# Optimization experiments

Hardware: AMD Instinct MI355X
Metric: run time of the kernel (lower is better)

Reference implementation:

```python
import jax, jax.numpy as jnp
import numpy as np

D_MODEL = 1024
NHEAD = 16
HEAD_DIM = D_MODEL // NHEAD
MLP_DIM = 4096
ROPE_THETA = 10000.0


def layer_norm(x, g, b, eps=1e-5):
    mu = jnp.mean(x, axis=-1, keepdims=True)
    var = jnp.var(x, axis=-1, keepdims=True)
    return (x - mu) * jax.lax.rsqrt(var + eps) * g + b


def rope_cos_sin(seq_len, dim):
    # lucidrains RotaryEmbedding: inv_freq over even indices, freqs repeated interleaved
    inv_freq = 1.0 / (ROPE_THETA ** (jnp.arange(0, dim, 2, dtype=jnp.float32) / dim))
    t = jnp.arange(seq_len, dtype=jnp.float32)
    freqs = t[:, None] * inv_freq[None, :]            # (S, dim/2)
    freqs = jnp.repeat(freqs, 2, axis=-1)             # (S, dim) interleaved [f0,f0,f1,f1,...]
    return jnp.cos(freqs), jnp.sin(freqs)


def apply_rope(x, cos, sin):
    # x: (B, S, H, D); interleaved rotate_half: (x0,x1) -> (-x1, x0)
    x1 = x[..., ::2]
    x2 = x[..., 1::2]
    rot = jnp.stack([-x2, x1], axis=-1).reshape(x.shape)
    c = cos[None, :, None, :]
    s = sin[None, :, None, :]
    return x * c + rot * s


def setup_inputs() -> dict:
    key = jax.random.key(0)
    ks = jax.random.split(key, 8)
    B, S = 2, 2048
    sc = 1.0 / np.sqrt(D_MODEL)
    inputs = jax.random.normal(ks[0], (B, S, D_MODEL), dtype=jnp.float32)
    return {
        "inputs": inputs,
        "ln1_g": jnp.ones((D_MODEL,), jnp.float32),
        "ln1_b": jnp.zeros((D_MODEL,), jnp.float32),
        "Wq": jax.random.normal(ks[1], (D_MODEL, D_MODEL), jnp.float32) * sc,
        "Wk": jax.random.normal(ks[2], (D_MODEL, D_MODEL), jnp.float32) * sc,
        "Wv": jax.random.normal(ks[3], (D_MODEL, D_MODEL), jnp.float32) * sc,
        "Wo": jax.random.normal(ks[4], (D_MODEL, D_MODEL), jnp.float32) * sc,
        "ln2_g": jnp.ones((D_MODEL,), jnp.float32),
        "ln2_b": jnp.zeros((D_MODEL,), jnp.float32),
        "Wfc2": jax.random.normal(ks[5], (D_MODEL, MLP_DIM), jnp.float32) * sc,
        "bfc2": jnp.zeros((MLP_DIM,), jnp.float32),
        "Wfc3": jax.random.normal(ks[6], (MLP_DIM, D_MODEL), jnp.float32) * (1.0 / np.sqrt(MLP_DIM)),
        "bfc3": jnp.zeros((D_MODEL,), jnp.float32),
    }


def reference(inputs, ln1_g, ln1_b, Wq, Wk, Wv, Wo, ln2_g, ln2_b, Wfc2, bfc2, Wfc3, bfc3):
    B, S, _ = inputs.shape
    x = layer_norm(inputs, ln1_g, ln1_b)
    q = (x @ Wq).reshape(B, S, NHEAD, HEAD_DIM)
    k = (x @ Wk).reshape(B, S, NHEAD, HEAD_DIM)
    v = (x @ Wv).reshape(B, S, NHEAD, HEAD_DIM)
    cos, sin = rope_cos_sin(S, HEAD_DIM)
    q = apply_rope(q, cos, sin)
    k = apply_rope(k, cos, sin)
    scores = jnp.einsum('bqhd,bkhd->bhqk', q, k) / np.sqrt(HEAD_DIM)
    attn = jax.nn.softmax(scores, axis=-1)
    out = jnp.einsum('bhqk,bkhd->bqhd', attn, v).reshape(B, S, D_MODEL)
    out = out @ Wo
    mlp_in = out + inputs
    h = layer_norm(mlp_in, ln2_g, ln2_b)
    h = jax.nn.gelu(h @ Wfc2 + bfc2, approximate=False)
    h = h @ Wfc3 + bfc3
    return h + mlp_in
```

## Files before the change

### kernel.cpp

```cpp
#include <hip/hip_runtime.h>
#include <cstdint>
#include <cstddef>

typedef __bf16 bf16x8 __attribute__((ext_vector_type(8)));
typedef __bf16 bf16x4 __attribute__((ext_vector_type(4)));
typedef float  f32x4  __attribute__((ext_vector_type(4)));
typedef float  f32x16 __attribute__((ext_vector_type(16)));

__device__ __forceinline__ void load16_to_lds(const void* g, void* l) {
  __builtin_amdgcn_global_load_lds(
      (const __attribute__((address_space(1))) void*)g,
      (__attribute__((address_space(3))) void*)l, 16, 0, 0);
}

__global__ __launch_bounds__(256) void transpose_cast(
    const float* __restrict__ src, __bf16* __restrict__ dst, int K, int N)
{
  __shared__ float tile[32][33];
  const int n0 = blockIdx.x * 32, k0 = blockIdx.y * 32;
  const int tx = threadIdx.x, ty = threadIdx.y;
#pragma unroll
  for (int i = 0; i < 32; i += 8)
    tile[ty + i][tx] = src[(size_t)(k0 + ty + i) * N + n0 + tx];
  __syncthreads();
#pragma unroll
  for (int i = 0; i < 32; i += 8)
    dst[(size_t)(n0 + ty + i) * K + k0 + tx] = (__bf16)tile[tx][ty + i];
}

__global__ __launch_bounds__(256) void transpose_cast_qkv(
    const float* __restrict__ s0, const float* __restrict__ s1,
    const float* __restrict__ s2, __bf16* __restrict__ dst)
{
  __shared__ float tile[32][33];
  const float* src = blockIdx.z == 0 ? s0 : blockIdx.z == 1 ? s1 : s2;
  __bf16* d = dst + (size_t)blockIdx.z * 1024 * 1024;
  const int n0 = blockIdx.x * 32, k0 = blockIdx.y * 32;
  const int tx = threadIdx.x, ty = threadIdx.y;
#pragma unroll
  for (int i = 0; i < 32; i += 8)
    tile[ty + i][tx] = src[(size_t)(k0 + ty + i) * 1024 + n0 + tx];
  __syncthreads();
#pragma unroll
  for (int i = 0; i < 32; i += 8)
    d[(size_t)(n0 + ty + i) * 1024 + k0 + tx] = (__bf16)tile[tx][ty + i];
}

__global__ __launch_bounds__(256) void ln_kernel(
    const float* __restrict__ x, const float* __restrict__ g,
    const float* __restrict__ bta, __bf16* __restrict__ out)
{
  const int row = blockIdx.x;
  const int t = threadIdx.x;
  const float4 v = ((const float4*)(x + (size_t)row * 1024))[t];
  float s  = v.x + v.y + v.z + v.w;
  float ss = v.x * v.x + v.y * v.y + v.z * v.z + v.w * v.w;
#pragma unroll
  for (int o = 32; o > 0; o >>= 1) { s += __shfl_down(s, o); ss += __shfl_down(ss, o); }
  __shared__ float rs[4], rss[4];
  const int w = t >> 6, l = t & 63;
  if (l == 0) { rs[w] = s; rss[w] = ss; }
  __syncthreads();
  s  = rs[0] + rs[1] + rs[2] + rs[3];
  ss = rss[0] + rss[1] + rss[2] + rss[3];
  const float mu = s * (1.0f / 1024.0f);
  const float var = ss * (1.0f / 1024.0f) - mu * mu;
  const float rstd = rsqrtf(var + 1e-5f);
  const float4 gg = ((const float4*)g)[t];
  const float4 bb = ((const float4*)bta)[t];
  __bf16* o = out + (size_t)row * 1024 + t * 4;
  o[0] = (__bf16)((v.x - mu) * rstd * gg.x + bb.x);
  o[1] = (__bf16)((v.y - mu) * rstd * gg.y + bb.y);
  o[2] = (__bf16)((v.z - mu) * rstd * gg.z + bb.z);
  o[3] = (__bf16)((v.w - mu) * rstd * gg.w + bb.w);
}

enum { EPI_BF16 = 0, EPI_RES_F32 = 1, EPI_GELU_BF16 = 2, EPI_BIAS_RES_F32 = 3 };

template <int TM, int KB, int EPI>
__global__ __launch_bounds__(256, 2) void gemm_bf16(
    const __bf16* __restrict__ A, const __bf16* __restrict__ Bt,
    __bf16* __restrict__ outb, float* __restrict__ outf,
    const float* __restrict__ bias, const float* __restrict__ res,
    int M, int N, int K)
{
  constexpr int MT = TM / 32;
  constexpr int KS = KB / 32;
  __shared__ __bf16 As0[TM * KB], As1[TM * KB];
  __shared__ __bf16 Bs0[128 * KB], Bs1[128 * KB];
  const int tid  = threadIdx.x;
  const int lane = tid & 63, w = tid >> 6;
  const int wm = w >> 1, wn = w & 1;
  const int quad = lane >> 4, l16 = lane & 15;
  const int m0 = blockIdx.y * TM, n0 = blockIdx.x * 128;

  f32x4 acc[MT][4] = {};
  const __bf16* Ag = A  + (size_t)m0 * K;
  const __bf16* Bg = Bt + (size_t)n0 * K;

#define G_STAGE(AsX, BsX, k0) {                                            \
    _Pragma("unroll")                                                      \
    for (int r2 = 0; r2 < TM * KB / 2048; ++r2) {                          \
      const int c = r2 * 256 + tid;                                        \
      const int r = c / (KB / 8), cb = c % (KB / 8);                       \
      const int g = (KB == 64) ? (cb ^ (r & 7)) : cb;                      \
      load16_to_lds(Ag + (size_t)r * K + (k0) + g * 8, &AsX[c * 8]);       \
    }                                                                      \
    _Pragma("unroll")                                                      \
    for (int r2 = 0; r2 < KB / 16; ++r2) {                                 \
      const int c = r2 * 256 + tid;                                        \
      const int r = c / (KB / 8), cb = c % (KB / 8);                       \
      const int g = (KB == 64) ? (cb ^ (r & 7)) : cb;                      \
      load16_to_lds(Bg + (size_t)r * K + (k0) + g * 8, &BsX[c * 8]);       \
    } }

#define G_COMPUTE(AsX, BsX) {                                              \
    bf16x8 af[MT][KS], bfr[4][KS];                                         \
    _Pragma("unroll")                                                      \
    for (int mt = 0; mt < MT; ++mt) {                                      \
      const int row = wm * (TM / 2) + mt * 16 + l16;                       \
      _Pragma("unroll")                                                    \
      for (int ks = 0; ks < KS; ++ks) {                                    \
        const int ch = (KB == 64) ? ((ks * 4 + quad) ^ (row & 7)) : quad;  \
        af[mt][ks] = *(const bf16x8*)&AsX[row * KB + ch * 8];              \
      }                                                                    \
    }                                                                      \
    _Pragma("unroll")                                                      \
    for (int nt = 0; nt < 4; ++nt) {                                       \
      const int row = wn * 64 + nt * 16 + l16;                             \
      _Pragma("unroll")                                                    \
      for (int ks = 0; ks < KS; ++ks) {                                    \
        const int ch = (KB == 64) ? ((ks * 4 + quad) ^ (row & 7)) : quad;  \
        bfr[nt][ks] = *(const bf16x8*)&BsX[row * KB + ch * 8];             \
      }                                                                    \
    }                                                                      \
    _Pragma("unroll")                                                      \
    for (int ks = 0; ks < KS; ++ks)                                        \
      _Pragma("unroll")                                                    \
      for (int mt = 0; mt < MT; ++mt)                                      \
        _Pragma("unroll")                                                  \
        for (int nt = 0; nt < 4; ++nt)                                     \
          acc[mt][nt] = __builtin_amdgcn_mfma_f32_16x16x32_bf16(           \
              af[mt][ks], bfr[nt][ks], acc[mt][nt], 0, 0, 0);              \
  }

  G_STAGE(As0, Bs0, 0);
  const int nk = K / KB;
  for (int kt = 0; kt < nk; kt += 2) {
    __syncthreads();
    if (kt + 1 < nk) G_STAGE(As1, Bs1, (kt + 1) * KB);
    G_COMPUTE(As0, Bs0);
    __syncthreads();
    if (kt + 2 < nk) G_STAGE(As0, Bs0, (kt + 2) * KB);
    G_COMPUTE(As1, Bs1);
  }
#undef G_STAGE
#undef G_COMPUTE

#pragma unroll
  for (int mt = 0; mt < MT; ++mt) {
#pragma unroll
    for (int nt = 0; nt < 4; ++nt) {
      const int col = n0 + wn * 64 + nt * 16 + l16;
#pragma unroll
      for (int i = 0; i < 4; ++i) {
        const int row = m0 + wm * (TM / 2) + mt * 16 + quad * 4 + i;
        float v = acc[mt][nt][i];
        const size_t idx = (size_t)row * N + col;
        if (EPI == EPI_BF16) {
          outb[idx] = (__bf16)v;
        } else if (EPI == EPI_RES_F32) {
          outf[idx] = v + res[idx];
        } else if (EPI == EPI_GELU_BF16) {
          v += bias[col];
          outb[idx] = (__bf16)(0.5f * v * (1.0f + erff(v * 0.70710678118f)));
        } else {
          v += bias[col];
          outf[idx] = v + res[idx];
        }
      }
    }
  }
}

__global__ __launch_bounds__(256) void rope_qk(
    const __bf16* __restrict__ qkv, __bf16* __restrict__ qr, __bf16* __restrict__ kr)
{
  const int idx = blockIdx.x * 256 + threadIdx.x;
  const int d2 = idx & 31;
  const int h  = (idx >> 5) & 15;
  const int bs = idx >> 9;
  const int s  = bs & 2047;
  const int b  = bs >> 11;
  const float inv_freq = exp2f(-((float)d2 * (1.0f / 32.0f)) * 13.2877123795f);
  const float ang = (float)s * inv_freq;
  const float c = cosf(ang), sn = sinf(ang);
  const float QS = 0.125f * 1.44269504f;
  const __bf16* qp = qkv + (size_t)bs * 3072 + h * 64 + 2 * d2;
  const __bf16* kp = qp + 1024;
  const float q0 = (float)qp[0], q1 = (float)qp[1];
  const float k0 = (float)kp[0], k1 = (float)kp[1];
  const size_t o = ((size_t)(b * 16 + h) * 2048 + s) * 64 + 2 * d2;
  qr[o]     = (__bf16)((q0 * c - q1 * sn) * QS);
  qr[o + 1] = (__bf16)((q1 * c + q0 * sn) * QS);
  kr[o]     = (__bf16)(k0 * c - k1 * sn);
  kr[o + 1] = (__bf16)(k1 * c + k0 * sn);
}

__global__ __launch_bounds__(256) void v_transpose(
    const __bf16* __restrict__ qkv, __bf16* __restrict__ vt)
{
  __shared__ __bf16 t[64][72];
  const int st = blockIdx.x, h = blockIdx.y, b = blockIdx.z;
  const int tx = threadIdx.x & 63, ty = threadIdx.x >> 6;
  const int s0 = st * 64;
  const __bf16* src = qkv + ((size_t)(b * 2048 + s0)) * 3072 + 2048 + h * 64;
#pragma unroll
  for (int i = 0; i < 64; i += 4)
    t[ty + i][tx] = src[(size_t)(ty + i) * 3072 + tx];
  __syncthreads();
  __bf16* dst = vt + ((size_t)(b * 16 + h) * 64) * 2048 + s0;
#pragma unroll
  for (int i = 0; i < 64; i += 4)
    dst[(size_t)(ty + i) * 2048 + tx] = t[tx][ty + i];
}

__global__ __launch_bounds__(256, 2) void attn_kernel(
    const __bf16* __restrict__ qr, const __bf16* __restrict__ kr,
    const __bf16* __restrict__ vt, __bf16* __restrict__ attn_o)
{
  constexpr int S = 2048, DH = 64, NH = 16, BQ = 128, BKK = 64;
  __shared__ __align__(16) __bf16 Qs[BQ * 64];
  __shared__ __align__(16) __bf16 Ks0[64 * 64], Ks1[64 * 64];
  __shared__ __align__(16) __bf16 Vts0[64 * 64], Vts1[64 * 64];

  const int tid = threadIdx.x;
  const int lane = tid & 63, w = tid >> 6;
  const int l32 = lane & 31, half = lane >> 5;
  const int qt = blockIdx.x, h = blockIdx.y, b = blockIdx.z;
  const int bh = b * NH + h;
  const __bf16* Q  = qr + ((size_t)bh * S + qt * BQ) * DH;
  const __bf16* Kp = kr + (size_t)bh * S * DH;
  const __bf16* Vp = vt + (size_t)bh * DH * S;
  __bf16* Pb = Qs + w * 2048;

#define A_STAGE(KsX, VtsX, kk) {                                           \
    _Pragma("unroll")                                                      \
    for (int r2 = 0; r2 < 2; ++r2) {                                       \
      const int c = r2 * 256 + tid;                                        \
      const int r = c >> 3, cb = c & 7;                                    \
      const int cg = (cb ^ (r & 7)) * 8;                                   \
      load16_to_lds(Kp + (size_t)((kk) + r) * DH + cg, &KsX[c * 8]);       \
      load16_to_lds(Vp + (size_t)r * S + (kk) + cg, &VtsX[c * 8]);         \
    } }

#pragma unroll
  for (int r4 = 0; r4 < 4; ++r4) {
    const int c = r4 * 256 + tid;
    const int r = c >> 3, cb = c & 7;
    load16_to_lds(Q + (size_t)r * DH + ((cb ^ (r & 7)) * 8), &Qs[c * 8]);
  }
  A_STAGE(Ks0, Vts0, 0);
  __syncthreads();

  bf16x8 qfB[4];
  {
    const int row = w * 32 + l32;
#pragma unroll
    for (int c = 0; c < 4; ++c)
      qfB[c] = *(const bf16x8*)&Qs[row * 64 + (((2 * c + half) ^ (row & 7)) * 8)];
  }

  float mreg = -3.0e38f, lreg = 0.0f;
  f32x16 oacc[2] = {};

#define A_COMPUTE(KsX, VtsX) {                                             \
    bf16x8 kf[2][4], vf[2][4];                                             \
    _Pragma("unroll")                                                      \
    for (int t = 0; t < 2; ++t) {                                          \
      const int row = 32 * t + l32;                                        \
      _Pragma("unroll")                                                    \
      for (int c = 0; c < 4; ++c)                                          \
        kf[t][c] = *(const bf16x8*)&KsX[row * 64 + (((2 * c + half) ^ (l32 & 7)) * 8)]; \
    }                                                                      \
    _Pragma("unroll")                                                      \
    for (int v = 0; v < 2; ++v) {                                          \
      const int row = 32 * v + l32;                                        \
      _Pragma("unroll")                                                    \
      for (int c = 0; c < 4; ++c)                                          \
        vf[v][c] = *(const bf16x8*)&VtsX[row * 64 + (((2 * c + half) ^ (l32 & 7)) * 8)]; \
    }                                                                      \
    f32x16 sa[2] = {};                                                     \
    _Pragma("unroll")                                                      \
    for (int t = 0; t < 2; ++t)                                            \
      _Pragma("unroll")                                                    \
      for (int c = 0; c < 4; ++c)                                          \
        sa[t] = __builtin_amdgcn_mfma_f32_32x32x16_bf16(kf[t][c], qfB[c], sa[t], 0, 0, 0); \
    float mx = -3.0e38f;                                                   \
    _Pragma("unroll")                                                      \
    for (int t = 0; t < 2; ++t)                                            \
      _Pragma("unroll")                                                    \
      for (int r = 0; r < 16; ++r) mx = fmaxf(mx, sa[t][r]);               \
    mx = fmaxf(mx, __shfl_xor(mx, 32));                                    \
    const float mnew = fmaxf(mreg, mx);                                    \
    const float alpha = __builtin_amdgcn_exp2f(mreg - mnew);               \
    mreg = mnew;                                                           \
    float sum = 0.0f;                                                      \
    _Pragma("unroll")                                                      \
    for (int t = 0; t < 2; ++t)                                            \
      _Pragma("unroll")                                                    \
      for (int r = 0; r < 16; ++r) {                                       \
        const float p = __builtin_amdgcn_exp2f(sa[t][r] - mnew);           \
        sa[t][r] = p;                                                      \
        sum += p;                                                          \
      }                                                                    \
    sum += __shfl_xor(sum, 32);                                            \
    lreg = lreg * alpha + sum;                                             \
    _Pragma("unroll")                                                      \
    for (int v = 0; v < 2; ++v)                                            \
      _Pragma("unroll")                                                    \
      for (int r = 0; r < 16; ++r) oacc[v][r] *= alpha;                    \
    _Pragma("unroll")                                                      \
    for (int t = 0; t < 2; ++t)                                            \
      _Pragma("unroll")                                                    \
      for (int g = 0; g < 4; ++g) {                                        \
        bf16x4 pv;                                                         \
        _Pragma("unroll")                                                  \
        for (int i = 0; i < 4; ++i) pv[i] = (__bf16)sa[t][4 * g + i];      \
        const int kc = 4 * t + g;                                          \
        *(bf16x4*)&Pb[l32 * 64 + ((kc ^ (l32 & 7)) * 8) + 4 * half] = pv;  \
      }                                                                    \
    bf16x8 pf[4];                                                          \
    _Pragma("unroll")                                                      \
    for (int c = 0; c < 4; ++c)                                            \
      pf[c] = *(const bf16x8*)&Pb[l32 * 64 + (((2 * c + half) ^ (l32 & 7)) * 8)]; \
    _Pragma("unroll")                                                      \
    for (int v = 0; v < 2; ++v)                                            \
      _Pragma("unroll")                                                    \
      for (int c = 0; c < 4; ++c)                                          \
        oacc[v] = __builtin_amdgcn_mfma_f32_32x32x16_bf16(vf[v][c], pf[c], oacc[v], 0, 0, 0); \
  }

  for (int kt = 0; kt < S / BKK; kt += 2) {
    __syncthreads();
    if (kt + 1 < S / BKK) A_STAGE(Ks1, Vts1, (kt + 1) * BKK);
    A_COMPUTE(Ks0, Vts0);
    __syncthreads();
    if (kt + 2 < S / BKK) A_STAGE(Ks0, Vts0, (kt + 2) * BKK);
    A_COMPUTE(Ks1, Vts1);
  }
#undef A_STAGE
#undef A_COMPUTE

  const float linv = 1.0f / lreg;
#pragma unroll
  for (int v = 0; v < 2; ++v)
#pragma unroll
    for (int g = 0; g < 4; ++g) {
      bf16x4 ov;
#pragma unroll
      for (int i = 0; i < 4; ++i) ov[i] = (__bf16)(oacc[v][4 * g + i] * linv);
      const int dc = 4 * v + g;
      *(bf16x4*)&Pb[l32 * 64 + ((dc ^ (l32 & 7)) * 8) + 4 * half] = ov;
    }
#pragma unroll
  for (int cc = 0; cc < 4; ++cc) {
    const int c = cc * 64 + lane;
    const int r = c >> 3, g = c & 7;
    const bf16x8 od = *(const bf16x8*)&Pb[r * 64 + ((g ^ (r & 7)) * 8)];
    const int srow = qt * BQ + w * 32 + r;
    *(bf16x8*)&attn_o[((size_t)b * S + srow) * 1024 + h * 64 + g * 8] = od;
  }
}

extern "C" void kernel_launch(void* const* d_in, const int* in_sizes, int n_in,
                              void* d_out, int out_size, void* d_ws, size_t ws_size,
                              hipStream_t stream) {
  const float* inputs = (const float*)d_in[0];
  const float* ln1_g  = (const float*)d_in[1];
  const float* ln1_b  = (const float*)d_in[2];
  const float* Wq     = (const float*)d_in[3];
  const float* Wk     = (const float*)d_in[4];
  const float* Wv     = (const float*)d_in[5];
  const float* Wo     = (const float*)d_in[6];
  const float* ln2_g  = (const float*)d_in[7];
  const float* ln2_b  = (const float*)d_in[8];
  const float* Wfc2   = (const float*)d_in[9];
  const float* bfc2   = (const float*)d_in[10];
  const float* Wfc3   = (const float*)d_in[11];
  const float* bfc3   = (const float*)d_in[12];
  float* out = (float*)d_out;
  char* ws = (char*)d_ws;
  const size_t MB = 1024 * 1024;

  __bf16* Wqkv_t = (__bf16*)(ws);
  __bf16* Wo_t   = (__bf16*)(ws + 6 * MB);
  __bf16* Wfc2_t = (__bf16*)(ws + 8 * MB);
  __bf16* Wfc3_t = (__bf16*)(ws + 16 * MB);
  __bf16* xb     = (__bf16*)(ws + 24 * MB);
  __bf16* attn_o = xb;
  __bf16* qkv    = (__bf16*)(ws + 32 * MB);
  float*  mlp_in = (float*)(ws + 32 * MB);
  __bf16* h2     = (__bf16*)(ws + 48 * MB);
  __bf16* qrb    = (__bf16*)(ws + 56 * MB);
  __bf16* krb    = (__bf16*)(ws + 64 * MB);
  __bf16* vtb    = (__bf16*)(ws + 72 * MB);
  __bf16* hbuf   = (__bf16*)(ws + 56 * MB);

  const dim3 tb(32, 8);
  transpose_cast_qkv<<<dim3(32, 32, 3), tb, 0, stream>>>(Wq, Wk, Wv, Wqkv_t);
  transpose_cast<<<dim3(32, 32),  tb, 0, stream>>>(Wo,   Wo_t,   1024, 1024);
  transpose_cast<<<dim3(128, 32), tb, 0, stream>>>(Wfc2, Wfc2_t, 1024, 4096);
  transpose_cast<<<dim3(32, 128), tb, 0, stream>>>(Wfc3, Wfc3_t, 4096, 1024);

  ln_kernel<<<4096, 256, 0, stream>>>(inputs, ln1_g, ln1_b, xb);

  gemm_bf16<128, 32, EPI_BF16><<<dim3(24, 32), 256, 0, stream>>>(
      xb, Wqkv_t, qkv, nullptr, nullptr, nullptr, 4096, 3072, 1024);

  rope_qk<<<8192, 256, 0, stream>>>(qkv, qrb, krb);
  v_transpose<<<dim3(32, 16, 2), 256, 0, stream>>>(qkv, vtb);

  attn_kernel<<<dim3(16, 16, 2), 256, 0, stream>>>(qrb, krb, vtb, attn_o);

  gemm_bf16<64, 64, EPI_RES_F32><<<dim3(8, 64), 256, 0, stream>>>(
      attn_o, Wo_t, nullptr, mlp_in, nullptr, inputs, 4096, 1024, 1024);

  ln_kernel<<<4096, 256, 0, stream>>>(mlp_in, ln2_g, ln2_b, h2);

  gemm_bf16<128, 32, EPI_GELU_BF16><<<dim3(32, 32), 256, 0, stream>>>(
      h2, Wfc2_t, hbuf, nullptr, bfc2, nullptr, 4096, 4096, 1024);

  gemm_bf16<64, 64, EPI_BIAS_RES_F32><<<dim3(8, 64), 256, 0, stream>>>(
      hbuf, Wfc3_t, nullptr, out, bfc3, mlp_in, 4096, 1024, 4096);
}
```

Before: 344.9 us.

## Keep attention P in registers via permlane32 swap, lazy rescale, setprio

In the attention inner loop, the P tile no longer round-trips through LDS. Probabilities are packed to bf16 with v_cvt_pk_bf16_f32 and rearranged across lanes with v_permlane32_swap so they feed the PV MFMA directly. Rescaling of the output accumulator and running sum is skipped unless some lane's block max exceeds the running max by more than 8 (log2 domain). The max and sum reductions use trees and split accumulators, and s_setprio is raised around the MFMA blocks. This removes LDS writes and reads plus a dependency per tile. The lazy rescale lets exp values grow up to 2^8, which could slightly affect bf16 precision.

```diff
diff --git a/kernel.cpp b/kernel.cpp
--- a/kernel.cpp
+++ b/kernel.cpp
@@ -6,11 +6,21 @@
 typedef __bf16 bf16x4 __attribute__((ext_vector_type(4)));
 typedef float  f32x4  __attribute__((ext_vector_type(4)));
 typedef float  f32x16 __attribute__((ext_vector_type(16)));
+typedef unsigned int u32x4 __attribute__((ext_vector_type(4)));
 
 __device__ __forceinline__ void load16_to_lds(const void* g, void* l) {
   __builtin_amdgcn_global_load_lds(
       (const __attribute__((address_space(1))) void*)g,
       (__attribute__((address_space(3))) void*)l, 16, 0, 0);
+}
+
+__device__ __forceinline__ unsigned cvt_pk_bf16(float a, float b) {
+  unsigned r;
+  asm("v_cvt_pk_bf16_f32 %0, %1, %2" : "=v"(r) : "v"(a), "v"(b));
+  return r;
+}
+__device__ __forceinline__ void permlane32_swap(unsigned &a, unsigned &b) {
+  asm("v_permlane32_swap_b32 %0, %1" : "+v"(a), "+v"(b));
 }
 
 __global__ __launch_bounds__(256) void transpose_cast(
@@ -291,54 +301,66 @@
         vf[v][c] = *(const bf16x8*)&VtsX[row * 64 + (((2 * c + half) ^ (l32 & 7)) * 8)]; \
     }                                                                      \
     f32x16 sa[2] = {};                                                     \
+    __builtin_amdgcn_s_setprio(1);                                         \
     _Pragma("unroll")                                                      \
     for (int t = 0; t < 2; ++t)                                            \
       _Pragma("unroll")                                                    \
       for (int c = 0; c < 4; ++c)                                          \
         sa[t] = __builtin_amdgcn_mfma_f32_32x32x16_bf16(kf[t][c], qfB[c], sa[t], 0, 0, 0); \
-    float mx = -3.0e38f;                                                   \
+    __builtin_amdgcn_s_setprio(0);                                         \
+    float pm[8];                                                           \
     _Pragma("unroll")                                                      \
     for (int t = 0; t < 2; ++t)                                            \
       _Pragma("unroll")                                                    \
-      for (int r = 0; r < 16; ++r) mx = fmaxf(mx, sa[t][r]);               \
+      for (int g = 0; g < 4; ++g)                                          \
+        pm[t * 4 + g] = fmaxf(fmaxf(sa[t][4 * g], sa[t][4 * g + 1]),       \
+                              fmaxf(sa[t][4 * g + 2], sa[t][4 * g + 3]));  \
+    float mx = fmaxf(fmaxf(fmaxf(pm[0], pm[1]), fmaxf(pm[2], pm[3])),      \
+                     fmaxf(fmaxf(pm[4], pm[5]), fmaxf(pm[6], pm[7])));     \
     mx = fmaxf(mx, __shfl_xor(mx, 32));                                    \
-    const float mnew = fmaxf(mreg, mx);                                    \
-    const float alpha = __builtin_amdgcn_exp2f(mreg - mnew);               \
-    mreg = mnew;                                                           \
-    float sum = 0.0f;                                                      \
+    float mnew = mreg;                                                     \
+    if (!__all(mx <= mreg + 8.0f)) {                                       \
+      mnew = fmaxf(mreg, mx);                                              \
+      const float alpha = __builtin_amdgcn_exp2f(mreg - mnew);             \
+      mreg = mnew;                                                         \
+      lreg *= alpha;                                                       \
+      _Pragma("unroll")                                                    \
+      for (int v = 0; v < 2; ++v)                                          \
+        _Pragma("unroll")                                                  \
+        for (int r = 0; r < 16; ++r) oacc[v][r] *= alpha;                  \
+    }                                                                      \
+    float ps0 = 0.f, ps1 = 0.f, ps2 = 0.f, ps3 = 0.f;                      \
     _Pragma("unroll")                                                      \
     for (int t = 0; t < 2; ++t)                                            \
       _Pragma("unroll")                                                    \
-      for (int r = 0; r < 16; ++r) {                                       \
-        const float p = __builtin_amdgcn_exp2f(sa[t][r] - mnew);           \
-        sa[t][r] = p;                                                      \
-        sum += p;                                                          \
+      for (int r = 0; r < 16; r += 4) {                                    \
+        const float p0 = __builtin_amdgcn_exp2f(sa[t][r]     - mnew);      \
+        const float p1 = __builtin_amdgcn_exp2f(sa[t][r + 1] - mnew);      \
+        const float p2 = __builtin_amdgcn_exp2f(sa[t][r + 2] - mnew);      \
+        const float p3 = __builtin_amdgcn_exp2f(sa[t][r + 3] - mnew);      \
+        sa[t][r] = p0; sa[t][r + 1] = p1;                                  \
+        sa[t][r + 2] = p2; sa[t][r + 3] = p3;                              \
+        ps0 += p0; ps1 += p1; ps2 += p2; ps3 += p3;                        \
       }                                                                    \
+    float sum = (ps0 + ps1) + (ps2 + ps3);                                 \
     sum += __shfl_xor(sum, 32);                                            \
-    lreg = lreg * alpha + sum;                                             \
-    _Pragma("unroll")                                                      \
-    for (int v = 0; v < 2; ++v)                                            \
-      _Pragma("unroll")                                                    \
-      for (int r = 0; r < 16; ++r) oacc[v][r] *= alpha;                    \
-    _Pragma("unroll")                                                      \
-    for (int t = 0; t < 2; ++t)                                            \
-      _Pragma("unroll")                                                    \
-      for (int g = 0; g < 4; ++g) {                                        \
-        bf16x4 pv;                                                         \
-        _Pragma("unroll")                                                  \
-        for (int i = 0; i < 4; ++i) pv[i] = (__bf16)sa[t][4 * g + i];      \
-        const int kc = 4 * t + g;                                          \
-        *(bf16x4*)&Pb[l32 * 64 + ((kc ^ (l32 & 7)) * 8) + 4 * half] = pv;  \
-      }                                                                    \
-    bf16x8 pf[4];                                                          \
-    _Pragma("unroll")                                                      \
-    for (int c = 0; c < 4; ++c)                                            \
-      pf[c] = *(const bf16x8*)&Pb[l32 * 64 + (((2 * c + half) ^ (l32 & 7)) * 8)]; \
-    _Pragma("unroll")                                                      \
-    for (int v = 0; v < 2; ++v)                                            \
-      _Pragma("unroll")                                                    \
-      for (int c = 0; c < 4; ++c)                                          \
-        oacc[v] = __builtin_amdgcn_mfma_f32_32x32x16_bf16(vf[v][c], pf[c], oacc[v], 0, 0, 0); \
+    lreg += sum;                                                           \
+    __builtin_amdgcn_s_setprio(1);                                         \
+    _Pragma("unroll")                                                      \
+    for (int c = 0; c < 4; ++c) {                                          \
+      const int t = c >> 1, r0 = (c & 1) * 8;                              \
+      unsigned px = cvt_pk_bf16(sa[t][r0],     sa[t][r0 + 1]);             \
+      unsigned py = cvt_pk_bf16(sa[t][r0 + 2], sa[t][r0 + 3]);             \
+      unsigned pz = cvt_pk_bf16(sa[t][r0 + 4], sa[t][r0 + 5]);             \
+      unsigned pw = cvt_pk_bf16(sa[t][r0 + 6], sa[t][r0 + 7]);             \
+      permlane32_swap(px, pz);                                             \
+      permlane32_swap(py, pw);                                             \
+      const u32x4 pv4 = { px, py, pz, pw };                                \
+      const bf16x8 pf = __builtin_bit_cast(bf16x8, pv4);                   \
+      oacc[0] = __builtin_amdgcn_mfma_f32_32x32x16_bf16(vf[0][c], pf, oacc[0], 0, 0, 0); \
+      oacc[1] = __builtin_amdgcn_mfma_f32_32x32x16_bf16(vf[1][c], pf, oacc[1], 0, 0, 0); \
+    }                                                                      \
+    __builtin_amdgcn_s_setprio(0);                                         \
   }
 
   for (int kt = 0; kt < S / BKK; kt += 2) {
```

Measured after the change: 343.7 us. Within noise of the previous version (-0.3%).
